# Performance work log

Hardware: AMD Instinct MI355X
Metric: run time of the kernel (lower is better)

Reference implementation:

```python
import jax, jax.numpy as jnp
import numpy as np

B, N, IN_DIM, OUT_DIM = 8, 2048, 128, 128
NEG_SLOPE = 0.2

def setup_inputs() -> dict:
    key = jax.random.key(0)
    k1, k2, k3, k4 = jax.random.split(key, 4)
    x = jax.random.normal(k1, (B, N, IN_DIM), dtype=jnp.float32)
    adj = jax.random.randint(k2, (N, N), 0, 2, dtype=jnp.int32)
    # nn.Linear weight init scale ~ 1/sqrt(fan_in)
    W = jax.random.normal(k3, (IN_DIM, OUT_DIM), dtype=jnp.float32) / np.sqrt(IN_DIM)
    a_vec = jax.random.normal(k4, (2 * OUT_DIM,), dtype=jnp.float32) / np.sqrt(2 * OUT_DIM)
    return {"x": x, "adj": adj, "W": W, "a_vec": a_vec}

def reference(x, adj, W, a_vec):
    # h = x @ W : [b, n, d]
    h = jnp.einsum("bni,io->bno", x, W)
    # Algebraic decomposition of a([h_i, h_j]) = a1.h_i + a2.h_j
    a1, a2 = a_vec[:OUT_DIM], a_vec[OUT_DIM:]
    s_i = h @ a1  # [b, n] score contribution from source node i
    s_j = h @ a2  # [b, n] score contribution from target node j
    e = s_i[:, :, None] + s_j[:, None, :]  # [b, n, n]
    e = jnp.where(e >= 0, e, NEG_SLOPE * e)  # leaky_relu(0.2)
    mask = (adj > 0)[None, :, :]  # [1, n, n] broadcast over batch
    e = jnp.where(mask, e, -jnp.inf)
    alpha = jax.nn.softmax(e, axis=-1)  # [b, n, n]
    out = jnp.einsum("bnm,bmd->bnd", alpha, h)  # [b, n, d]
    return out, alpha
```

## Files before the change

kernel.cpp:

```cpp
#include <hip/hip_runtime.h>
#include <hip/hip_bf16.h>
#include <cstdint>
#include <cstddef>

constexpr int Bn = 8;
constexpr int Nn = 2048;
constexpr int Dn = 128;

typedef __bf16 bf16x8 __attribute__((ext_vector_type(8)));
typedef float f32x4 __attribute__((ext_vector_type(4)));

#define AS1 __attribute__((address_space(1)))
#define AS3 __attribute__((address_space(3)))

static __device__ __forceinline__ void gl_lds16(const void* g, void* l) {
  __builtin_amdgcn_global_load_lds((AS1 const void*)g, (AS3 void*)l, 16, 0, 0);
}

__global__ __launch_bounds__(256) void gat_k1(
    const float* __restrict__ x, const float* __restrict__ W,
    const float* __restrict__ a_vec,
    __bf16* __restrict__ hT, float* __restrict__ s1, float* __restrict__ s2) {
  __shared__ __align__(16) float Wl[64 * 144];
  __shared__ __align__(16) float xL[32 * 132];

  const int t = threadIdx.x;
  const int r0 = blockIdx.x * 32;
  const int b = r0 >> 11;
  const int n0 = r0 & (Nn - 1);
  const int rp = (t >> 4) << 1;
  const int c0 = (t & 15) << 3;
  const int c0p = c0 + ((c0 >> 5) << 2);

  float acc[2][8];
#pragma unroll
  for (int r = 0; r < 2; ++r)
#pragma unroll
    for (int c = 0; c < 8; ++c) acc[r][c] = 0.f;

#pragma unroll
  for (int it = 0; it < 4; ++it) {
    int idx = t + (it << 8);
    int rr = idx >> 5, kc = (idx & 31) << 2;
    *(float4*)(xL + rr * 132 + kc) = *(const float4*)(x + (size_t)(r0 + rr) * Dn + kc);
  }

  for (int ph = 0; ph < 2; ++ph) {
    if (ph) __syncthreads();
#pragma unroll
    for (int it = 0; it < 8; ++it) {
      int idx = t + (it << 8);
      int kk = idx >> 5, c4 = (idx & 31) << 2;
      int dsto = kk * 144 + c4 + ((c4 >> 5) << 2);
      *(float4*)(Wl + dsto) = *(const float4*)(W + (size_t)((ph << 6) + kk) * Dn + c4);
    }
    __syncthreads();
    const float* xrow = xL + rp * 132 + (ph << 6);
    for (int k = 0; k < 64; ++k) {
      float xa0 = xrow[k];
      float xa1 = xrow[132 + k];
      float4 w0 = *(const float4*)(Wl + k * 144 + c0p);
      float4 w1 = *(const float4*)(Wl + k * 144 + c0p + 4);
      float ws[8] = {w0.x, w0.y, w0.z, w0.w, w1.x, w1.y, w1.z, w1.w};
#pragma unroll
      for (int c = 0; c < 8; ++c) {
        acc[0][c] = fmaf(xa0, ws[c], acc[0][c]);
        acc[1][c] = fmaf(xa1, ws[c], acc[1][c]);
      }
    }
  }

  float q1[2] = {0.f, 0.f}, q2[2] = {0.f, 0.f};
#pragma unroll
  for (int c = 0; c < 8; ++c) {
    float a1c = a_vec[c0 + c];
    float a2c = a_vec[Dn + c0 + c];
    q1[0] = fmaf(acc[0][c], a1c, q1[0]);
    q1[1] = fmaf(acc[1][c], a1c, q1[1]);
    q2[0] = fmaf(acc[0][c], a2c, q2[0]);
    q2[1] = fmaf(acc[1][c], a2c, q2[1]);
  }
#pragma unroll
  for (int d = 1; d < 16; d <<= 1) {
    q1[0] += __shfl_xor(q1[0], d);
    q1[1] += __shfl_xor(q1[1], d);
    q2[0] += __shfl_xor(q2[0], d);
    q2[1] += __shfl_xor(q2[1], d);
  }
  if ((t & 15) == 0) {
    s1[b * Nn + n0 + rp] = q1[0];
    s1[b * Nn + n0 + rp + 1] = q1[1];
    s2[b * Nn + n0 + rp] = q2[0];
    s2[b * Nn + n0 + rp + 1] = q2[1];
  }

#pragma unroll
  for (int c = 0; c < 8; ++c) {
    union { __bf16 h[2]; uint32_t u; } pk;
    pk.h[0] = (__bf16)acc[0][c];
    pk.h[1] = (__bf16)acc[1][c];
    *(uint32_t*)(hT + (size_t)(b * Dn + c0 + c) * Nn + n0 + rp) = pk.u;
  }
}

__global__ __launch_bounds__(512) void gat_k2(
    const int* __restrict__ adj, const __bf16* __restrict__ hT,
    const float* __restrict__ s1, const float* __restrict__ s2,
    float* __restrict__ out, float* __restrict__ alpha) {
  __shared__ __align__(16) float sj[Nn];
  __shared__ float siv[32], invl[32];
  __shared__ __align__(16) __bf16 Pl[2][32 * 72];
  __shared__ __align__(16) __bf16 hl[2][128 * 64];

  const int t = threadIdx.x;
  const int b = blockIdx.x >> 6;
  const int i0 = (blockIdx.x & 63) << 5;
  const int w = t >> 6, lane = t & 63;
  const int ii = t >> 4, sub = t & 15;
  const int lrow = lane >> 3, ccs = lane & 7;
  const __bf16* __restrict__ hTb = hT + (size_t)b * Dn * Nn;

#pragma unroll
  for (int inst = 0; inst < 2; ++inst) {
    int row = (w << 4) + (inst << 3) + lrow;
    gl_lds16(hTb + (size_t)row * Nn + ((ccs ^ lrow) << 3),
             &hl[0][((w << 4) + (inst << 3)) << 6]);
  }

  *(float4*)(sj + (t << 2)) = *(const float4*)(s2 + b * Nn + (t << 2));
  if (t < 32) siv[t] = s1[b * Nn + i0 + t];
  __syncthreads();

  const int i = i0 + ii;
  const int* __restrict__ adjrow = adj + (size_t)i * Nn;
  const float si = siv[ii];

  float l = 0.f;
  uint32_t mb0 = 0, mb1 = 0, mb2 = 0, mb3 = 0;
#define PASS1_G(G, MW)                                                        \
  {                                                                           \
    _Pragma("unroll")                                                         \
    for (int u = 0; u < 8; ++u) {                                             \
      int j = (((G) << 3) + u) * 64 + (sub << 2);                             \
      int4 am = *(const int4*)(adjrow + j);                                   \
      float4 sv = *(const float4*)(sj + j);                                   \
      float e0 = si + sv.x; e0 = fmaxf(e0, 0.2f * e0);                        \
      float e1 = si + sv.y; e1 = fmaxf(e1, 0.2f * e1);                        \
      float e2 = si + sv.z; e2 = fmaxf(e2, 0.2f * e2);                        \
      float e3 = si + sv.w; e3 = fmaxf(e3, 0.2f * e3);                        \
      l += (am.x > 0) ? __expf(e0) : 0.f;                                     \
      l += (am.y > 0) ? __expf(e1) : 0.f;                                     \
      l += (am.z > 0) ? __expf(e2) : 0.f;                                     \
      l += (am.w > 0) ? __expf(e3) : 0.f;                                     \
      uint32_t mbt = (am.x > 0 ? 1u : 0u) | (am.y > 0 ? 2u : 0u) |            \
                     (am.z > 0 ? 4u : 0u) | (am.w > 0 ? 8u : 0u);             \
      MW |= mbt << (u << 2);                                                  \
    }                                                                         \
  }
  PASS1_G(0, mb0)
  PASS1_G(1, mb1)
  PASS1_G(2, mb2)
  PASS1_G(3, mb3)
#undef PASS1_G

  l += __shfl_xor(l, 1);
  l += __shfl_xor(l, 2);
  l += __shfl_xor(l, 4);
  l += __shfl_xor(l, 8);
  if (sub == 0) invl[ii] = 1.f / l;
  __syncthreads();
  const float il = invl[ii];

  const int iw = (w & 1) << 4;
  const int nd0 = (w >> 1) << 5;
  const int q16 = lane >> 4, m16 = lane & 15;
  f32x4 acc0 = {0.f, 0.f, 0.f, 0.f}, acc1 = {0.f, 0.f, 0.f, 0.f};
  float* __restrict__ arow = alpha + ((size_t)(b * Nn + i) << 11);

  for (int g = 0; g < 4; ++g) {
    const uint32_t mw = (g & 2) ? ((g & 1) ? mb3 : mb2) : ((g & 1) ? mb1 : mb0);
#pragma unroll
    for (int u = 0; u < 8; ++u) {
      const int buf = u & 1;
      const int j0r = (g << 9) + (u << 6);
      {
        int j = j0r + (sub << 2);
        float4 sv = *(const float4*)(sj + j);
        float e0 = si + sv.x; e0 = fmaxf(e0, 0.2f * e0);
        float e1 = si + sv.y; e1 = fmaxf(e1, 0.2f * e1);
        float e2 = si + sv.z; e2 = fmaxf(e2, 0.2f * e2);
        float e3 = si + sv.w; e3 = fmaxf(e3, 0.2f * e3);
        float a0 = (mw & (1u << ((u << 2) + 0))) ? __expf(e0) * il : 0.f;
        float a1 = (mw & (1u << ((u << 2) + 1))) ? __expf(e1) * il : 0.f;
        float a2 = (mw & (1u << ((u << 2) + 2))) ? __expf(e2) * il : 0.f;
        float a3 = (mw & (1u << ((u << 2) + 3))) ? __expf(e3) * il : 0.f;
        f32x4 av = {a0, a1, a2, a3};
        __builtin_nontemporal_store(av, (f32x4*)(arow + j));
        union { __bf16 h[4]; uint2 u2; } pk;
        pk.h[0] = (__bf16)a0; pk.h[1] = (__bf16)a1;
        pk.h[2] = (__bf16)a2; pk.h[3] = (__bf16)a3;
        *(uint2*)(&Pl[buf][ii * 72 + (sub << 2)]) = pk.u2;
      }
      asm volatile("s_waitcnt vmcnt(1) lgkmcnt(0)\n\ts_barrier" ::: "memory");
      if (u < 7 || g < 3) {
        int jn = j0r + 64;
#pragma unroll
        for (int inst = 0; inst < 2; ++inst) {
          int row = (w << 4) + (inst << 3) + lrow;
          gl_lds16(hTb + (size_t)row * Nn + jn + ((ccs ^ lrow) << 3),
                   &hl[buf ^ 1][((w << 4) + (inst << 3)) << 6]);
        }
      }
      __builtin_amdgcn_sched_barrier(0);
#pragma unroll
      for (int ks = 0; ks < 2; ++ks) {
        bf16x8 af = *(const bf16x8*)(&Pl[buf][(iw + m16) * 72 + (ks << 5) + (q16 << 3)]);
        {
          int d = nd0 + m16;
          int phys = ((ks << 2) + q16) ^ (d & 7);
          bf16x8 bv = *(const bf16x8*)(&hl[buf][(d << 6) + (phys << 3)]);
          acc0 = __builtin_amdgcn_mfma_f32_16x16x32_bf16(af, bv, acc0, 0, 0, 0);
        }
        {
          int d = nd0 + 16 + m16;
          int phys = ((ks << 2) + q16) ^ (d & 7);
          bf16x8 bv = *(const bf16x8*)(&hl[buf][(d << 6) + (phys << 3)]);
          acc1 = __builtin_amdgcn_mfma_f32_16x16x32_bf16(af, bv, acc1, 0, 0, 0);
        }
      }
    }
  }

#pragma unroll
  for (int nb = 0; nb < 2; ++nb) {
    f32x4 a = nb ? acc1 : acc0;
    int d = nd0 + (nb << 4) + m16;
#pragma unroll
    for (int r = 0; r < 4; ++r) {
      int irow = i0 + iw + (q16 << 2) + r;
      out[((size_t)(b * Nn + irow) << 7) + d] = a[r];
    }
  }
}

extern "C" void kernel_launch(void* const* d_in, const int* in_sizes, int n_in,
                              void* d_out, int out_size, void* d_ws, size_t ws_size,
                              hipStream_t stream) {
  const float* x = (const float*)d_in[0];
  const int* adj = (const int*)d_in[1];
  const float* W = (const float*)d_in[2];
  const float* a_vec = (const float*)d_in[3];

  float* out = (float*)d_out;
  float* alpha = out + (size_t)Bn * Nn * Dn;

  char* ws = (char*)d_ws;
  __bf16* hT = (__bf16*)ws;
  float* s1 = (float*)(ws + (size_t)Bn * Dn * Nn * 2);
  float* s2 = s1 + (size_t)Bn * Nn;

  gat_k1<<<512, 256, 0, stream>>>(x, W, a_vec, hT, s1, s2);
  gat_k2<<<512, 512, 0, stream>>>(adj, hT, s1, s2, out, alpha);
}
```

Before: 192.8 us.

## Triple-buffer hT tiles and software-pipeline alpha compute with MFMA

Replaces the double-buffered hT staging with a three-slot ring buffer and restructures the inner loop into a software pipeline. The softmax/alpha computation for tile k+1 now runs in the same barrier interval as the MFMA on tile k, with prefetch two tiles ahead. The aim is to hide global-to-LDS load latency and overlap exp/store work with matrix ops while needing fewer stalls per tile. The cost is 16KB more LDS per block, which may reduce the number of resident blocks per CU, and a more fragile vmcnt accounting that mixes the alpha stores with the LDS loads.

```diff
diff --git a/kernel.cpp b/kernel.cpp
--- a/kernel.cpp
+++ b/kernel.cpp
@@ -110,7 +110,7 @@
   __shared__ __align__(16) float sj[Nn];
   __shared__ float siv[32], invl[32];
   __shared__ __align__(16) __bf16 Pl[2][32 * 72];
-  __shared__ __align__(16) __bf16 hl[2][128 * 64];
+  __shared__ __align__(16) __bf16 hl[3 * 128 * 64];
 
   const int t = threadIdx.x;
   const int b = blockIdx.x >> 6;
@@ -124,7 +124,7 @@
   for (int inst = 0; inst < 2; ++inst) {
     int row = (w << 4) + (inst << 3) + lrow;
     gl_lds16(hTb + (size_t)row * Nn + ((ccs ^ lrow) << 3),
-             &hl[0][((w << 4) + (inst << 3)) << 6]);
+             &hl[((w << 4) + (inst << 3)) << 6]);
   }
 
   *(float4*)(sj + (t << 2)) = *(const float4*)(s2 + b * Nn + (t << 2));
@@ -177,59 +177,75 @@
   f32x4 acc0 = {0.f, 0.f, 0.f, 0.f}, acc1 = {0.f, 0.f, 0.f, 0.f};
   float* __restrict__ arow = alpha + ((size_t)(b * Nn + i) << 11);
 
-  for (int g = 0; g < 4; ++g) {
-    const uint32_t mw = (g & 2) ? ((g & 1) ? mb3 : mb2) : ((g & 1) ? mb1 : mb0);
-#pragma unroll
-    for (int u = 0; u < 8; ++u) {
-      const int buf = u & 1;
-      const int j0r = (g << 9) + (u << 6);
+  auto alpha_phase = [&](int k, int parity) {
+    int j = (k << 6) + (sub << 2);
+    float4 sv = *(const float4*)(sj + j);
+    uint32_t mw = (k & 16) ? ((k & 8) ? mb3 : mb2) : ((k & 8) ? mb1 : mb0);
+    int sh = (k & 7) << 2;
+    float e0 = si + sv.x; e0 = fmaxf(e0, 0.2f * e0);
+    float e1 = si + sv.y; e1 = fmaxf(e1, 0.2f * e1);
+    float e2 = si + sv.z; e2 = fmaxf(e2, 0.2f * e2);
+    float e3 = si + sv.w; e3 = fmaxf(e3, 0.2f * e3);
+    float a0 = ((mw >> (sh + 0)) & 1u) ? __expf(e0) * il : 0.f;
+    float a1 = ((mw >> (sh + 1)) & 1u) ? __expf(e1) * il : 0.f;
+    float a2 = ((mw >> (sh + 2)) & 1u) ? __expf(e2) * il : 0.f;
+    float a3 = ((mw >> (sh + 3)) & 1u) ? __expf(e3) * il : 0.f;
+    f32x4 av = {a0, a1, a2, a3};
+    __builtin_nontemporal_store(av, (f32x4*)(arow + j));
+    union { __bf16 h[4]; uint2 u2; } pk;
+    pk.h[0] = (__bf16)a0; pk.h[1] = (__bf16)a1;
+    pk.h[2] = (__bf16)a2; pk.h[3] = (__bf16)a3;
+    *(uint2*)(&Pl[parity][ii * 72 + (sub << 2)]) = pk.u2;
+  };
+
+  auto mfma_phase = [&](int parity, const __bf16* hb) {
+#pragma unroll
+    for (int ks = 0; ks < 2; ++ks) {
+      bf16x8 af = *(const bf16x8*)(&Pl[parity][(iw + m16) * 72 + (ks << 5) + (q16 << 3)]);
       {
-        int j = j0r + (sub << 2);
-        float4 sv = *(const float4*)(sj + j);
-        float e0 = si + sv.x; e0 = fmaxf(e0, 0.2f * e0);
-        float e1 = si + sv.y; e1 = fmaxf(e1, 0.2f * e1);
-        float e2 = si + sv.z; e2 = fmaxf(e2, 0.2f * e2);
-        float e3 = si + sv.w; e3 = fmaxf(e3, 0.2f * e3);
-        float a0 = (mw & (1u << ((u << 2) + 0))) ? __expf(e0) * il : 0.f;
-        float a1 = (mw & (1u << ((u << 2) + 1))) ? __expf(e1) * il : 0.f;
-        float a2 = (mw & (1u << ((u << 2) + 2))) ? __expf(e2) * il : 0.f;
-        float a3 = (mw & (1u << ((u << 2) + 3))) ? __expf(e3) * il : 0.f;
-        f32x4 av = {a0, a1, a2, a3};
-        __builtin_nontemporal_store(av, (f32x4*)(arow + j));
-        union { __bf16 h[4]; uint2 u2; } pk;
-        pk.h[0] = (__bf16)a0; pk.h[1] = (__bf16)a1;
-        pk.h[2] = (__bf16)a2; pk.h[3] = (__bf16)a3;
-        *(uint2*)(&Pl[buf][ii * 72 + (sub << 2)]) = pk.u2;
+        int d = nd0 + m16;
+        int phys = ((ks << 2) + q16) ^ (d & 7);
+        bf16x8 bv = *(const bf16x8*)(&hb[(d << 6) + (phys << 3)]);
+        acc0 = __builtin_amdgcn_mfma_f32_16x16x32_bf16(af, bv, acc0, 0, 0, 0);
       }
-      asm volatile("s_waitcnt vmcnt(1) lgkmcnt(0)\n\ts_barrier" ::: "memory");
-      if (u < 7 || g < 3) {
-        int jn = j0r + 64;
-#pragma unroll
-        for (int inst = 0; inst < 2; ++inst) {
-          int row = (w << 4) + (inst << 3) + lrow;
-          gl_lds16(hTb + (size_t)row * Nn + jn + ((ccs ^ lrow) << 3),
-                   &hl[buf ^ 1][((w << 4) + (inst << 3)) << 6]);
-        }
+      {
+        int d = nd0 + 16 + m16;
+        int phys = ((ks << 2) + q16) ^ (d & 7);
+        bf16x8 bv = *(const bf16x8*)(&hb[(d << 6) + (phys << 3)]);
+        acc1 = __builtin_amdgcn_mfma_f32_16x16x32_bf16(af, bv, acc1, 0, 0, 0);
       }
-      __builtin_amdgcn_sched_barrier(0);
-#pragma unroll
-      for (int ks = 0; ks < 2; ++ks) {
-        bf16x8 af = *(const bf16x8*)(&Pl[buf][(iw + m16) * 72 + (ks << 5) + (q16 << 3)]);
-        {
-          int d = nd0 + m16;
-          int phys = ((ks << 2) + q16) ^ (d & 7);
-          bf16x8 bv = *(const bf16x8*)(&hl[buf][(d << 6) + (phys << 3)]);
-          acc0 = __builtin_amdgcn_mfma_f32_16x16x32_bf16(af, bv, acc0, 0, 0, 0);
-        }
-        {
-          int d = nd0 + 16 + m16;
-          int phys = ((ks << 2) + q16) ^ (d & 7);
-          bf16x8 bv = *(const bf16x8*)(&hl[buf][(d << 6) + (phys << 3)]);
-          acc1 = __builtin_amdgcn_mfma_f32_16x16x32_bf16(af, bv, acc1, 0, 0, 0);
-        }
-      }
-    }
-  }
+    }
+  };
+
+  auto stage = [&](int jn, int bidx) {
+#pragma unroll
+    for (int inst = 0; inst < 2; ++inst) {
+      int row = (w << 4) + (inst << 3) + lrow;
+      gl_lds16(hTb + (size_t)row * Nn + jn + ((ccs ^ lrow) << 3),
+               &hl[(bidx << 13) + (((w << 4) + (inst << 3)) << 6)]);
+    }
+  };
+
+  stage(64, 1);
+  __builtin_amdgcn_sched_barrier(0);
+  alpha_phase(0, 0);
+  asm volatile("s_waitcnt lgkmcnt(0)\n\ts_barrier" ::: "memory");
+
+  int bi = 0;
+  for (int jt = 0; jt < 30; ++jt) {
+    int bp = bi + 2;
+    if (bp >= 3) bp -= 3;
+    stage((jt + 2) << 6, bp);
+    __builtin_amdgcn_sched_barrier(0);
+    mfma_phase(jt & 1, &hl[bi << 13]);
+    alpha_phase(jt + 1, (jt + 1) & 1);
+    asm volatile("s_waitcnt vmcnt(4) lgkmcnt(0)\n\ts_barrier" ::: "memory");
+    bi = (bi == 2) ? 0 : bi + 1;
+  }
+  mfma_phase(0, &hl[0]);
+  alpha_phase(31, 1);
+  asm volatile("s_waitcnt vmcnt(2) lgkmcnt(0)\n\ts_barrier" ::: "memory");
+  mfma_phase(1, &hl[1 << 13]);
 
 #pragma unroll
   for (int nb = 0; nb < 2; ++nb) {
```

After: 213.4 us. +10.7%, slower.

## Pre-pack adjacency into bitmask kernel and reorder blocks batch-innermost

Applied to the files above, without the earlier changes.

Adds a small kernel that reads the int32 adjacency matrix once and packs it into a 1-bit-per-edge mask. The main attention kernel then loads four 32-bit words per thread instead of re-reading the full int32 adjacency row for each batch. This aims to remove the repeated adjacency traffic across the batch dimension. Block indexing is also changed so the batch index is innermost, which places blocks sharing the same rows next to each other. The cost is an extra kernel launch and one extra pass over adjacency.

```diff
diff --git a/kernel.cpp b/kernel.cpp
--- a/kernel.cpp
+++ b/kernel.cpp
@@ -103,8 +103,25 @@
   }
 }
 
+__global__ __launch_bounds__(256) void gat_kpack(
+    const int* __restrict__ adj, uint32_t* __restrict__ pkm) {
+  const int t = threadIdx.x;
+  const int row = (blockIdx.x << 2) + (t >> 6);
+  const int l = t & 63;
+  const int* __restrict__ ar = adj + (size_t)row * Nn + (l << 2);
+  uint32_t m = 0;
+#pragma unroll
+  for (int k = 0; k < 8; ++k) {
+    int4 a = *(const int4*)(ar + (k << 8));
+    uint32_t nib = (a.x > 0 ? 1u : 0u) | (a.y > 0 ? 2u : 0u) |
+                   (a.z > 0 ? 4u : 0u) | (a.w > 0 ? 8u : 0u);
+    m |= nib << (k << 2);
+  }
+  pkm[(row << 6) + l] = m;
+}
+
 __global__ __launch_bounds__(512) void gat_k2(
-    const int* __restrict__ adj, const __bf16* __restrict__ hT,
+    const uint32_t* __restrict__ pkm, const __bf16* __restrict__ hT,
     const float* __restrict__ s1, const float* __restrict__ s2,
     float* __restrict__ out, float* __restrict__ alpha) {
   __shared__ __align__(16) float sj[Nn];
@@ -113,8 +130,8 @@
   __shared__ __align__(16) __bf16 hl[2][128 * 64];
 
   const int t = threadIdx.x;
-  const int b = blockIdx.x >> 6;
-  const int i0 = (blockIdx.x & 63) << 5;
+  const int b = blockIdx.x & 7;
+  const int i0 = (blockIdx.x >> 3) << 5;
   const int w = t >> 6, lane = t & 63;
   const int ii = t >> 4, sub = t & 15;
   const int lrow = lane >> 3, ccs = lane & 7;
@@ -132,36 +149,33 @@
   __syncthreads();
 
   const int i = i0 + ii;
-  const int* __restrict__ adjrow = adj + (size_t)i * Nn;
   const float si = siv[ii];
 
+  const uint32_t* __restrict__ pk = pkm + ((size_t)i << 6);
+  const uint32_t pk0 = pk[sub];
+  const uint32_t pk1 = pk[sub + 16];
+  const uint32_t pk2 = pk[sub + 32];
+  const uint32_t pk3 = pk[sub + 48];
+
   float l = 0.f;
-  uint32_t mb0 = 0, mb1 = 0, mb2 = 0, mb3 = 0;
-#define PASS1_G(G, MW)                                                        \
-  {                                                                           \
-    _Pragma("unroll")                                                         \
-    for (int u = 0; u < 8; ++u) {                                             \
-      int j = (((G) << 3) + u) * 64 + (sub << 2);                             \
-      int4 am = *(const int4*)(adjrow + j);                                   \
-      float4 sv = *(const float4*)(sj + j);                                   \
-      float e0 = si + sv.x; e0 = fmaxf(e0, 0.2f * e0);                        \
-      float e1 = si + sv.y; e1 = fmaxf(e1, 0.2f * e1);                        \
-      float e2 = si + sv.z; e2 = fmaxf(e2, 0.2f * e2);                        \
-      float e3 = si + sv.w; e3 = fmaxf(e3, 0.2f * e3);                        \
-      l += (am.x > 0) ? __expf(e0) : 0.f;                                     \
-      l += (am.y > 0) ? __expf(e1) : 0.f;                                     \
-      l += (am.z > 0) ? __expf(e2) : 0.f;                                     \
-      l += (am.w > 0) ? __expf(e3) : 0.f;                                     \
-      uint32_t mbt = (am.x > 0 ? 1u : 0u) | (am.y > 0 ? 2u : 0u) |            \
-                     (am.z > 0 ? 4u : 0u) | (am.w > 0 ? 8u : 0u);             \
-      MW |= mbt << (u << 2);                                                  \
-    }                                                                         \
-  }
-  PASS1_G(0, mb0)
-  PASS1_G(1, mb1)
-  PASS1_G(2, mb2)
-  PASS1_G(3, mb3)
-#undef PASS1_G
+  for (int g = 0; g < 4; ++g) {
+    const int shg = g << 3;
+#pragma unroll
+    for (int u = 0; u < 8; ++u) {
+      int j = (((g << 3) + u) << 6) + (sub << 2);
+      float4 sv = *(const float4*)(sj + j);
+      uint32_t mw = (u & 2) ? ((u & 1) ? pk3 : pk2) : ((u & 1) ? pk1 : pk0);
+      int sh = shg + ((u >> 2) << 2);
+      float e0 = si + sv.x; e0 = fmaxf(e0, 0.2f * e0);
+      float e1 = si + sv.y; e1 = fmaxf(e1, 0.2f * e1);
+      float e2 = si + sv.z; e2 = fmaxf(e2, 0.2f * e2);
+      float e3 = si + sv.w; e3 = fmaxf(e3, 0.2f * e3);
+      l += ((mw >> (sh + 0)) & 1u) ? __expf(e0) : 0.f;
+      l += ((mw >> (sh + 1)) & 1u) ? __expf(e1) : 0.f;
+      l += ((mw >> (sh + 2)) & 1u) ? __expf(e2) : 0.f;
+      l += ((mw >> (sh + 3)) & 1u) ? __expf(e3) : 0.f;
+    }
+  }
 
   l += __shfl_xor(l, 1);
   l += __shfl_xor(l, 2);
@@ -178,7 +192,7 @@
   float* __restrict__ arow = alpha + ((size_t)(b * Nn + i) << 11);
 
   for (int g = 0; g < 4; ++g) {
-    const uint32_t mw = (g & 2) ? ((g & 1) ? mb3 : mb2) : ((g & 1) ? mb1 : mb0);
+    const int shg = g << 3;
 #pragma unroll
     for (int u = 0; u < 8; ++u) {
       const int buf = u & 1;
@@ -186,20 +200,22 @@
       {
         int j = j0r + (sub << 2);
         float4 sv = *(const float4*)(sj + j);
+        uint32_t mw = (u & 2) ? ((u & 1) ? pk3 : pk2) : ((u & 1) ? pk1 : pk0);
+        int sh = shg + ((u >> 2) << 2);
         float e0 = si + sv.x; e0 = fmaxf(e0, 0.2f * e0);
         float e1 = si + sv.y; e1 = fmaxf(e1, 0.2f * e1);
         float e2 = si + sv.z; e2 = fmaxf(e2, 0.2f * e2);
         float e3 = si + sv.w; e3 = fmaxf(e3, 0.2f * e3);
-        float a0 = (mw & (1u << ((u << 2) + 0))) ? __expf(e0) * il : 0.f;
-        float a1 = (mw & (1u << ((u << 2) + 1))) ? __expf(e1) * il : 0.f;
-        float a2 = (mw & (1u << ((u << 2) + 2))) ? __expf(e2) * il : 0.f;
-        float a3 = (mw & (1u << ((u << 2) + 3))) ? __expf(e3) * il : 0.f;
+        float a0 = ((mw >> (sh + 0)) & 1u) ? __expf(e0) * il : 0.f;
+        float a1 = ((mw >> (sh + 1)) & 1u) ? __expf(e1) * il : 0.f;
+        float a2 = ((mw >> (sh + 2)) & 1u) ? __expf(e2) * il : 0.f;
+        float a3 = ((mw >> (sh + 3)) & 1u) ? __expf(e3) * il : 0.f;
         f32x4 av = {a0, a1, a2, a3};
         __builtin_nontemporal_store(av, (f32x4*)(arow + j));
-        union { __bf16 h[4]; uint2 u2; } pk;
-        pk.h[0] = (__bf16)a0; pk.h[1] = (__bf16)a1;
-        pk.h[2] = (__bf16)a2; pk.h[3] = (__bf16)a3;
-        *(uint2*)(&Pl[buf][ii * 72 + (sub << 2)]) = pk.u2;
+        union { __bf16 h[4]; uint2 u2; } pkv;
+        pkv.h[0] = (__bf16)a0; pkv.h[1] = (__bf16)a1;
+        pkv.h[2] = (__bf16)a2; pkv.h[3] = (__bf16)a3;
+        *(uint2*)(&Pl[buf][ii * 72 + (sub << 2)]) = pkv.u2;
       }
       asm volatile("s_waitcnt vmcnt(1) lgkmcnt(0)\n\ts_barrier" ::: "memory");
       if (u < 7 || g < 3) {
@@ -258,7 +274,9 @@
   __bf16* hT = (__bf16*)ws;
   float* s1 = (float*)(ws + (size_t)Bn * Dn * Nn * 2);
   float* s2 = s1 + (size_t)Bn * Nn;
+  uint32_t* pkm = (uint32_t*)(s2 + (size_t)Bn * Nn);
 
   gat_k1<<<512, 256, 0, stream>>>(x, W, a_vec, hT, s1, s2);
-  gat_k2<<<512, 512, 0, stream>>>(adj, hT, s1, s2, out, alpha);
-}
+  gat_kpack<<<512, 256, 0, stream>>>(adj, pkm);
+  gat_k2<<<512, 512, 0, stream>>>(pkm, hT, s1, s2, out, alpha);
+}
```

After: 193.1 us. About the same (+0.1%).
